# Kernel tuning notes

Measured on AMD Instinct MI355X. Metric: run time of the kernel, lower is better.

Reference implementation:

```python
import jax, jax.numpy as jnp
import numpy as np

N_NODES = 100000
N_EDGES = 1600000
D_FEAT = 128
UNITS = 128
LEAKY_ALPHA = 0.2  # tf.nn.leaky_relu default


def setup_inputs() -> dict:
    key = jax.random.key(0)
    k1, k2, k3, k4 = jax.random.split(key, 4)
    node_states = jax.random.normal(k1, (N_NODES, D_FEAT), dtype=jnp.float32)
    edges = jax.random.randint(k2, (N_EDGES, 2), 0, N_NODES, dtype=jnp.int64)
    kernel = jax.random.normal(k3, (D_FEAT, UNITS), dtype=jnp.float32) * (1.0 / np.sqrt(D_FEAT))
    kernel_attention = jax.random.normal(k4, (2 * UNITS, 1), dtype=jnp.float32) * (1.0 / np.sqrt(2 * UNITS))
    return {
        "node_states": node_states,
        "edges": edges,
        "kernel": kernel,
        "kernel_attention": kernel_attention,
    }


def reference(node_states, edges, kernel, kernel_attention):
    n = node_states.shape[0]
    tgt_idx = edges[:, 0]
    src_idx = edges[:, 1]

    # node_states_transformed: [N, units]
    h = node_states @ kernel

    # Attention logits. concat([tgt, src]) @ ka == tgt @ ka_t + src @ ka_s
    # (avoids materializing the [E, 2*units] concat).
    ka_t = kernel_attention[:UNITS, 0]   # [units]
    ka_s = kernel_attention[UNITS:, 0]   # [units]
    score_t = h @ ka_t                   # [N]
    score_s = h @ ka_s                   # [N]
    e = score_t[tgt_idx] + score_s[src_idx]              # [E]
    e = jax.nn.leaky_relu(e, negative_slope=LEAKY_ALPHA)
    e = jnp.exp(jnp.clip(e, -2.0, 2.0))

    # Segment softmax over incoming edges of each target node.
    sum_e = jax.ops.segment_sum(e, tgt_idx, num_segments=n)  # [N]
    attention = e / (sum_e[tgt_idx] + 1e-9)                  # [E]

    # Weighted scatter-sum of source messages.
    messages = h[src_idx] * attention[:, None]               # [E, units]
    output = jax.ops.segment_sum(messages, tgt_idx, num_segments=n)  # [N, units]
    return output
```

## Files before the change

### kernel.cpp

```cpp
#include <hip/hip_runtime.h>
#include <stdint.h>

typedef unsigned short ushort_t;
typedef __attribute__((ext_vector_type(8))) short short8;
typedef __attribute__((ext_vector_type(4))) float float4v;
typedef __attribute__((ext_vector_type(2))) float float2v;

#define N_NODES 100000
#define N_EDGES 1600000
#define D 128
#define NB_GEMM 1563
#define NBP     782
#define NB_B1   250
#define EPB     6400
#define BUCKETS 782
#define CAP     2560

static __device__ __forceinline__ float2v up2(uint32_t u) {
    float2v r;
    r.x = __builtin_bit_cast(float, u << 16);
    r.y = __builtin_bit_cast(float, u & 0xffff0000u);
    return r;
}
static __device__ __forceinline__ uint32_t f2bf_u(float f) {
    uint32_t u = __builtin_bit_cast(uint32_t, f);
    return (u + 0x7fffu + ((u >> 16) & 1u)) >> 16;
}
static __device__ __forceinline__ ushort_t f2bf(float f) {
    return (ushort_t)f2bf_u(f);
}
static __device__ __forceinline__ uint32_t pack2(float a, float b) {
    return f2bf_u(a) | (f2bf_u(b) << 16);
}
static __device__ __forceinline__ float edge_e(float s) {
    float x = (s >= 0.0f) ? s : 0.2f * s;
    x = fminf(fmaxf(x, -2.0f), 2.0f);
    return __expf(x);
}

__global__ void __launch_bounds__(256) prep_kernel(const float* __restrict__ W,
                                                   const float* __restrict__ KA,
                                                   float* __restrict__ wa,
                                                   ushort_t* __restrict__ WT,
                                                   const int* __restrict__ E,
                                                   int* __restrict__ eflag) {
    __shared__ int s;
    int b = blockIdx.x, t = threadIdx.x;
    int i = b * 256 + t;
    if (b < 64) {
        int k = i >> 7, nn = i & 127;
        int kb = k >> 5, q = (k >> 3) & 3, j = k & 7;
        int tt = nn >> 4, l = nn & 15;
        WT[((kb * 8 + tt) * 64 + q * 16 + l) * 8 + j] = f2bf(W[i]);
    } else if (b == 64) {
        if (t == 0) s = 0;
        __syncthreads();
        int nz = 0;
#pragma unroll
        for (int j = 0; j < 8; j++)
            if (E[(t + j * 256) * 2 + 1] != 0) nz = 1;
        if (nz) atomicOr(&s, 1);
        __syncthreads();
        if (t == 0) *eflag = (s == 0) ? 1 : 0;
    } else if (b == 65) {
        int half = t >> 7, k = t & 127;
        const float* kav = KA + half * 128;
        const float* wrow = W + k * 128;
        float acc = 0.0f;
#pragma unroll 8
        for (int j = 0; j < 128; j++) acc += wrow[j] * kav[j];
        wa[half * 128 + k] = acc;
    }
}

__global__ void __launch_bounds__(256) mega1_kernel(const float* __restrict__ X,
                                                    const ushort_t* __restrict__ WT,
                                                    const float* __restrict__ wa,
                                                    ushort_t* __restrict__ H,
                                                    float* __restrict__ st,
                                                    float* __restrict__ ss,
                                                    int M,
                                                    const int* __restrict__ E,
                                                    const int* __restrict__ eflag,
                                                    int* __restrict__ sortedE,
                                                    ushort_t* __restrict__ bmat,
                                                    ushort_t* __restrict__ lofs) {
    __shared__ int lds_b1[1280];
    if (blockIdx.x >= NBP) {
        int eb = blockIdx.x - NBP;
        int t = threadIdx.x;
        int* lhist = lds_b1;
        int* lpart = lds_b1 + 1024;
        for (int j = t; j < 1024; j += 256) lhist[j] = 0;
        __syncthreads();
        int i64 = *eflag;
        int base = eb * EPB;
        for (int j = 0; j < 25; j++) {
            int i = base + j * 256 + t;
            int tgt = i64 ? E[i * 4] : E[i * 2];
            if ((unsigned)tgt >= (unsigned)N_NODES) tgt = 0;
            atomicAdd(&lhist[tgt >> 7], 1);
        }
        __syncthreads();
        int c0 = lhist[t * 4], c1 = lhist[t * 4 + 1];
        int c2 = lhist[t * 4 + 2], c3 = lhist[t * 4 + 3];
        int sum = c0 + c1 + c2 + c3;
        lpart[t] = sum;
        __syncthreads();
        for (int off = 1; off < 256; off <<= 1) {
            int x = (t >= off) ? lpart[t - off] : 0;
            __syncthreads();
            lpart[t] += x;
            __syncthreads();
        }
        int e0 = lpart[t] - sum;
        int e1 = e0 + c0, e2 = e1 + c1, e3 = e2 + c2;
        int cc[4] = {c0, c1, c2, c3};
        int ee[4] = {e0, e1, e2, e3};
#pragma unroll
        for (int k = 0; k < 4; k++) {
            int bb = t * 4 + k;
            if (bb < BUCKETS) {
                bmat[eb * BUCKETS + bb] = (ushort_t)cc[k];
                lofs[eb * BUCKETS + bb] = (ushort_t)ee[k];
            }
        }
        lhist[t * 4] = e0; lhist[t * 4 + 1] = e1;
        lhist[t * 4 + 2] = e2; lhist[t * 4 + 3] = e3;
        __syncthreads();
        for (int j = 0; j < 25; j++) {
            int i = base + j * 256 + t;
            int tgt, src;
            if (i64) { tgt = E[i * 4]; src = E[i * 4 + 2]; }
            else     { tgt = E[i * 2]; src = E[i * 2 + 1]; }
            if ((unsigned)tgt >= (unsigned)N_NODES) tgt = 0;
            if ((unsigned)src >= (unsigned)N_NODES) src = 0;
            int pos = atomicAdd(&lhist[tgt >> 7], 1);
            if (pos < EPB) sortedE[base + pos] = ((tgt & 127) << 17) | src;
        }
        return;
    }
    int tid = threadIdx.x;
    int wave = tid >> 6, lane = tid & 63;
    int quad = lane >> 4, l16 = lane & 15;
    const short8* Bf = (const short8*)WT;

    int t0 = blockIdx.x;
    int nt = (t0 + NBP < NB_GEMM) ? 2 : 1;

    float4 f[8];
    {
        int ar = t0 * 64 + wave * 16 + l16; if (ar >= M) ar = M - 1;
        const float* xr = X + (size_t)ar * D + quad * 8;
#pragma unroll
        for (int kb = 0; kb < 4; kb++) {
            f[kb * 2]     = *(const float4*)(xr + kb * 32);
            f[kb * 2 + 1] = *(const float4*)(xr + kb * 32 + 4);
        }
    }
    for (int it = 0; it < nt; it++) {
        int m0 = (t0 + it * NBP) * 64 + wave * 16;
        float4 nf[8];
        if (it + 1 < nt) {
            int ar = (t0 + NBP) * 64 + wave * 16 + l16; if (ar >= M) ar = M - 1;
            const float* xr = X + (size_t)ar * D + quad * 8;
#pragma unroll
            for (int kb = 0; kb < 4; kb++) {
                nf[kb * 2]     = *(const float4*)(xr + kb * 32);
                nf[kb * 2 + 1] = *(const float4*)(xr + kb * 32 + 4);
            }
        }
        short8 a[4];
        float sct = 0.0f, scs = 0.0f;
#pragma unroll
        for (int kb = 0; kb < 4; kb++) {
            float4 f0 = f[kb * 2], f1 = f[kb * 2 + 1];
            const float* wt0 = wa + kb * 32 + quad * 8;
            float4 t0v = *(const float4*)(wt0);
            float4 t1v = *(const float4*)(wt0 + 4);
            float4 s0v = *(const float4*)(wt0 + 128);
            float4 s1v = *(const float4*)(wt0 + 132);
            sct += f0.x * t0v.x + f0.y * t0v.y + f0.z * t0v.z + f0.w * t0v.w
                 + f1.x * t1v.x + f1.y * t1v.y + f1.z * t1v.z + f1.w * t1v.w;
            scs += f0.x * s0v.x + f0.y * s0v.y + f0.z * s0v.z + f0.w * s0v.w
                 + f1.x * s1v.x + f1.y * s1v.y + f1.z * s1v.z + f1.w * s1v.w;
            short8 v;
            v[0] = (short)f2bf(f0.x); v[1] = (short)f2bf(f0.y);
            v[2] = (short)f2bf(f0.z); v[3] = (short)f2bf(f0.w);
            v[4] = (short)f2bf(f1.x); v[5] = (short)f2bf(f1.y);
            v[6] = (short)f2bf(f1.z); v[7] = (short)f2bf(f1.w);
            a[kb] = v;
        }
        sct += __shfl_xor(sct, 16); sct += __shfl_xor(sct, 32);
        scs += __shfl_xor(scs, 16); scs += __shfl_xor(scs, 32);
        if (quad == 0 && m0 + l16 < M) { st[m0 + l16] = sct; ss[m0 + l16] = scs; }

        float4v acc[8] = {};
#pragma unroll
        for (int kb = 0; kb < 4; kb++) {
#pragma unroll
            for (int t = 0; t < 8; t++) {
                short8 b = Bf[(kb * 8 + t) * 64 + lane];
                acc[t] = __builtin_amdgcn_mfma_f32_16x16x32_bf16(a[kb], b, acc[t], 0, 0, 0);
            }
        }
#pragma unroll
        for (int r = 0; r < 4; r++) {
            int orow = m0 + quad * 4 + r;
            if (orow < M) {
                uint4 v;
                v.x = pack2(acc[0][r], acc[1][r]);
                v.y = pack2(acc[2][r], acc[3][r]);
                v.z = pack2(acc[4][r], acc[5][r]);
                v.w = pack2(acc[6][r], acc[7][r]);
                *(uint4*)(H + (size_t)orow * D + l16 * 8) = v;
            }
        }
        if (it + 1 < nt) {
#pragma unroll
            for (int j = 0; j < 8; j++) f[j] = nf[j];
        }
    }
}

__global__ void __launch_bounds__(512) agg2_kernel(const ushort_t* __restrict__ bmat,
                                                   const ushort_t* __restrict__ lofs,
                                                   const int* __restrict__ sortedE,
                                                   const float* __restrict__ st,
                                                   const float* __restrict__ ss,
                                                   const ushort_t* __restrict__ H,
                                                   float* __restrict__ out) {
    __shared__ int stage[CAP];
    __shared__ int sortedLoc[CAP];
    __shared__ int lh[128];
    __shared__ int lrp[129];
    __shared__ int wsum[8];
    int b = blockIdx.x, t = threadIdx.x;
    int lane = t & 63, wv = t >> 6;
    int cnt = 0, sst = 0;
    if (t < NB_B1) {
        cnt = bmat[t * BUCKETS + b];
        sst = lofs[t * BUCKETS + b];
    }
    int x = cnt;
#pragma unroll
    for (int off = 1; off < 64; off <<= 1) {
        int y = __shfl_up(x, off);
        if (lane >= off) x += y;
    }
    if (lane == 63) wsum[wv] = x;
    if (t < 128) lh[t] = 0;
    __syncthreads();
    int wbase = 0, total = 0;
#pragma unroll
    for (int w = 0; w < 8; w++) {
        int sv = wsum[w];
        if (w < wv) wbase += sv;
        total += sv;
    }
    if (total > CAP) total = CAP;
    int soff = wbase + x - cnt;
    for (int k = 0; k < cnt; k++) {
        int idx = soff + k;
        if (idx < CAP) stage[idx] = sortedE[t * EPB + sst + k];
    }
    __syncthreads();
    for (int j = t; j < total; j += 512)
        atomicAdd(&lh[stage[j] >> 17], 1);
    __syncthreads();
    int v = (t < 128) ? lh[t] : 0;
    int xs = v;
#pragma unroll
    for (int off = 1; off < 64; off <<= 1) {
        int y = __shfl_up(xs, off);
        if (lane >= off) xs += y;
    }
    if (t == 63) wsum[0] = xs;
    __syncthreads();
    if (t < 128) {
        int inc = (wv == 1) ? xs + wsum[0] : xs;
        int ex = inc - v;
        lrp[t] = ex;
        lh[t]  = ex;
    }
    if (t == 0) lrp[128] = total;
    __syncthreads();
    for (int j = t; j < total; j += 512) {
        int p = stage[j];
        int pos = atomicAdd(&lh[p >> 17], 1);
        if (pos < total) sortedLoc[pos] = p & 0x1FFFF;
    }
    __syncthreads();
    int g = lane >> 4, l = lane & 15;
    for (int nd = wv; nd < 128; nd += 8) {
        int gnode = b * 128 + nd;
        if (gnode >= N_NODES) break;
        int start = lrp[nd], end = lrp[nd + 1];
        float stn = st[gnode];
        float den = 0.0f;
        float2v acc2[4] = {};
        int m = start + g;
        for (; m + 4 < end; m += 8) {
            int s0 = sortedLoc[m], s1 = sortedLoc[m + 4];
            float e0 = edge_e(stn + ss[s0]);
            float e1 = edge_e(stn + ss[s1]);
            den += e0 + e1;
            uint4 p0 = *(const uint4*)(H + ((unsigned)s0 << 7) + l * 8);
            uint4 p1 = *(const uint4*)(H + ((unsigned)s1 << 7) + l * 8);
            float2v E0 = {e0, e0}, E1 = {e1, e1};
            acc2[0] += E0 * up2(p0.x) + E1 * up2(p1.x);
            acc2[1] += E0 * up2(p0.y) + E1 * up2(p1.y);
            acc2[2] += E0 * up2(p0.z) + E1 * up2(p1.z);
            acc2[3] += E0 * up2(p0.w) + E1 * up2(p1.w);
        }
        if (m < end) {
            int s0 = sortedLoc[m];
            float e0 = edge_e(stn + ss[s0]);
            den += e0;
            uint4 p0 = *(const uint4*)(H + ((unsigned)s0 << 7) + l * 8);
            float2v E0 = {e0, e0};
            acc2[0] += E0 * up2(p0.x);
            acc2[1] += E0 * up2(p0.y);
            acc2[2] += E0 * up2(p0.z);
            acc2[3] += E0 * up2(p0.w);
        }
        den += __shfl_xor(den, 16);
        den += __shfl_xor(den, 32);
        float r[8];
#pragma unroll
        for (int j = 0; j < 4; j++) {
            float a0 = acc2[j].x, a1 = acc2[j].y;
            a0 += __shfl_xor(a0, 16); a0 += __shfl_xor(a0, 32);
            a1 += __shfl_xor(a1, 16); a1 += __shfl_xor(a1, 32);
            r[j * 2] = a0; r[j * 2 + 1] = a1;
        }
        float inv = 1.0f / (den + 1e-9f);
        if (g == 0) {
#pragma unroll
            for (int k = 0; k < 8; k++)
                out[(size_t)gnode * D + k * 16 + l] = r[k] * inv;
        }
    }
}

extern "C" void kernel_launch(void* const* d_in, const int* in_sizes, int n_in,
                              void* d_out, int out_size, void* d_ws, size_t ws_size,
                              hipStream_t stream) {
    const float* X  = (const float*)d_in[0];
    const int*   E  = (const int*)d_in[1];
    const float* W  = (const float*)d_in[2];
    const float* KA = (const float*)d_in[3];
    for (int i = 0; i < n_in; i++) {
        int s = in_sizes[i];
        if (s == N_NODES * D)      X  = (const float*)d_in[i];
        else if (s == N_EDGES * 2) E  = (const int*)d_in[i];
        else if (s == D * D)       W  = (const float*)d_in[i];
        else if (s == 2 * D)       KA = (const float*)d_in[i];
    }
    float* out = (float*)d_out;

    char* ws = (char*)d_ws;
    ushort_t* H        = (ushort_t*)(ws + 0);
    float*    wa       = (float*)   (ws + 25600000);
    float*    st       = (float*)   (ws + 25601024);
    float*    ssb      = (float*)   (ws + 26001024);
    int*      sortedE  = (int*)     (ws + 26401024);
    ushort_t* bmat     = (ushort_t*)(ws + 32801024);
    ushort_t* lofs     = (ushort_t*)(ws + 33192032);
    int*      eflag    = (int*)     (ws + 33583040);
    ushort_t* WT       = (ushort_t*)(ws + 33583072);

    prep_kernel<<<66, 256, 0, stream>>>(W, KA, wa, WT, E, eflag);
    mega1_kernel<<<NBP + NB_B1, 256, 0, stream>>>(X, WT, wa, H, st, ssb,
                                                  N_NODES, E, eflag,
                                                  sortedE, bmat, lofs);
    agg2_kernel<<<BUCKETS, 512, 0, stream>>>(bmat, lofs, sortedE, st, ssb,
                                             H, out);
}
```

Before: 227.3 us.

## Split bucketing and GEMM kernels, stage weights in LDS, parallelize staging gather

Splits the fused edge-bucketing/GEMM kernel into two separate launches. The bucketing kernel now reads each edge once with vector loads and keeps bins in registers, and the GEMM stages the transposed weights in LDS. The aggregation kernel fills its staging buffer with one element per thread, finding the owning partition by binary search, and unrolls the gather loop to four edges. The split adds a launch and loses the overlap between bucketing and GEMM, and the larger LDS footprint may cut occupancy.

```diff
diff --git a/kernel.cpp b/kernel.cpp
--- a/kernel.cpp
+++ b/kernel.cpp
@@ -73,78 +73,83 @@
     }
 }
 
-__global__ void __launch_bounds__(256) mega1_kernel(const float* __restrict__ X,
-                                                    const ushort_t* __restrict__ WT,
-                                                    const float* __restrict__ wa,
-                                                    ushort_t* __restrict__ H,
-                                                    float* __restrict__ st,
-                                                    float* __restrict__ ss,
-                                                    int M,
-                                                    const int* __restrict__ E,
-                                                    const int* __restrict__ eflag,
-                                                    int* __restrict__ sortedE,
-                                                    ushort_t* __restrict__ bmat,
-                                                    ushort_t* __restrict__ lofs) {
-    __shared__ int lds_b1[1280];
-    if (blockIdx.x >= NBP) {
-        int eb = blockIdx.x - NBP;
-        int t = threadIdx.x;
-        int* lhist = lds_b1;
-        int* lpart = lds_b1 + 1024;
-        for (int j = t; j < 1024; j += 256) lhist[j] = 0;
+__global__ void __launch_bounds__(256) b1_kernel(const int* __restrict__ E,
+                                                 const int* __restrict__ eflag,
+                                                 int* __restrict__ sortedE,
+                                                 ushort_t* __restrict__ bmat,
+                                                 ushort_t* __restrict__ lofs) {
+    __shared__ int lhist[1024];
+    __shared__ int lpart[256];
+    int eb = blockIdx.x, t = threadIdx.x;
+    for (int j = t; j < 1024; j += 256) lhist[j] = 0;
+    __syncthreads();
+    int i64 = *eflag;
+    int base = eb * EPB;
+    int bin[25], w[25];
+#pragma unroll
+    for (int j = 0; j < 25; j++) {
+        int i = base + j * 256 + t;
+        int tgt, src;
+        if (i64) { uint4 v = *(const uint4*)(E + (size_t)i * 4); tgt = (int)v.x; src = (int)v.z; }
+        else     { uint2 v = *(const uint2*)(E + (size_t)i * 2); tgt = (int)v.x; src = (int)v.y; }
+        if ((unsigned)tgt >= (unsigned)N_NODES) tgt = 0;
+        if ((unsigned)src >= (unsigned)N_NODES) src = 0;
+        bin[j] = tgt >> 7;
+        w[j]   = ((tgt & 127) << 17) | src;
+        atomicAdd(&lhist[bin[j]], 1);
+    }
+    __syncthreads();
+    int c0 = lhist[t * 4], c1 = lhist[t * 4 + 1];
+    int c2 = lhist[t * 4 + 2], c3 = lhist[t * 4 + 3];
+    int sum = c0 + c1 + c2 + c3;
+    lpart[t] = sum;
+    __syncthreads();
+    for (int off = 1; off < 256; off <<= 1) {
+        int x = (t >= off) ? lpart[t - off] : 0;
         __syncthreads();
-        int i64 = *eflag;
-        int base = eb * EPB;
-        for (int j = 0; j < 25; j++) {
-            int i = base + j * 256 + t;
-            int tgt = i64 ? E[i * 4] : E[i * 2];
-            if ((unsigned)tgt >= (unsigned)N_NODES) tgt = 0;
-            atomicAdd(&lhist[tgt >> 7], 1);
-        }
+        lpart[t] += x;
         __syncthreads();
-        int c0 = lhist[t * 4], c1 = lhist[t * 4 + 1];
-        int c2 = lhist[t * 4 + 2], c3 = lhist[t * 4 + 3];
-        int sum = c0 + c1 + c2 + c3;
-        lpart[t] = sum;
-        __syncthreads();
-        for (int off = 1; off < 256; off <<= 1) {
-            int x = (t >= off) ? lpart[t - off] : 0;
-            __syncthreads();
-            lpart[t] += x;
-            __syncthreads();
-        }
-        int e0 = lpart[t] - sum;
-        int e1 = e0 + c0, e2 = e1 + c1, e3 = e2 + c2;
-        int cc[4] = {c0, c1, c2, c3};
-        int ee[4] = {e0, e1, e2, e3};
-#pragma unroll
-        for (int k = 0; k < 4; k++) {
-            int bb = t * 4 + k;
-            if (bb < BUCKETS) {
-                bmat[eb * BUCKETS + bb] = (ushort_t)cc[k];
-                lofs[eb * BUCKETS + bb] = (ushort_t)ee[k];
-            }
-        }
-        lhist[t * 4] = e0; lhist[t * 4 + 1] = e1;
-        lhist[t * 4 + 2] = e2; lhist[t * 4 + 3] = e3;
-        __syncthreads();
-        for (int j = 0; j < 25; j++) {
-            int i = base + j * 256 + t;
-            int tgt, src;
-            if (i64) { tgt = E[i * 4]; src = E[i * 4 + 2]; }
-            else     { tgt = E[i * 2]; src = E[i * 2 + 1]; }
-            if ((unsigned)tgt >= (unsigned)N_NODES) tgt = 0;
-            if ((unsigned)src >= (unsigned)N_NODES) src = 0;
-            int pos = atomicAdd(&lhist[tgt >> 7], 1);
-            if (pos < EPB) sortedE[base + pos] = ((tgt & 127) << 17) | src;
-        }
-        return;
-    }
+    }
+    int e0 = lpart[t] - sum;
+    int e1 = e0 + c0, e2 = e1 + c1, e3 = e2 + c2;
+    int cc[4] = {c0, c1, c2, c3};
+    int ee[4] = {e0, e1, e2, e3};
+#pragma unroll
+    for (int k = 0; k < 4; k++) {
+        int bb = t * 4 + k;
+        if (bb < BUCKETS) {
+            bmat[eb * BUCKETS + bb] = (ushort_t)cc[k];
+            lofs[eb * BUCKETS + bb] = (ushort_t)ee[k];
+        }
+    }
+    lhist[t * 4] = e0; lhist[t * 4 + 1] = e1;
+    lhist[t * 4 + 2] = e2; lhist[t * 4 + 3] = e3;
+    __syncthreads();
+#pragma unroll
+    for (int j = 0; j < 25; j++) {
+        int pos = atomicAdd(&lhist[bin[j]], 1);
+        if (pos < EPB) sortedE[base + pos] = w[j];
+    }
+}
+
+__global__ void __launch_bounds__(256) gemm_kernel(const float* __restrict__ X,
+                                                   const ushort_t* __restrict__ WT,
+                                                   const float* __restrict__ wa,
+                                                   ushort_t* __restrict__ H,
+                                                   float* __restrict__ st,
+                                                   float* __restrict__ ss,
+                                                   int M) {
+    __shared__ ushort_t lds_wt[16384];
     int tid = threadIdx.x;
+    {
+        const uint4* srcp = (const uint4*)WT;
+        uint4* dstp = (uint4*)lds_wt;
+        for (int j = tid; j < 2048; j += 256) dstp[j] = srcp[j];
+    }
+    __syncthreads();
+
     int wave = tid >> 6, lane = tid & 63;
     int quad = lane >> 4, l16 = lane & 15;
-    const short8* Bf = (const short8*)WT;
-
     int t0 = blockIdx.x;
     int nt = (t0 + NBP < NB_GEMM) ? 2 : 1;
 
@@ -200,7 +205,7 @@
         for (int kb = 0; kb < 4; kb++) {
 #pragma unroll
             for (int t = 0; t < 8; t++) {
-                short8 b = Bf[(kb * 8 + t) * 64 + lane];
+                short8 b = *(const short8*)(&lds_wt[((kb * 8 + t) * 64 + lane) * 8]);
                 acc[t] = __builtin_amdgcn_mfma_f32_16x16x32_bf16(a[kb], b, acc[t], 0, 0, 0);
             }
         }
@@ -235,6 +240,8 @@
     __shared__ int lh[128];
     __shared__ int lrp[129];
     __shared__ int wsum[8];
+    __shared__ int lsoff[NB_B1];
+    __shared__ int lsst[NB_B1];
     int b = blockIdx.x, t = threadIdx.x;
     int lane = t & 63, wv = t >> 6;
     int cnt = 0, sst = 0;
@@ -260,9 +267,15 @@
     }
     if (total > CAP) total = CAP;
     int soff = wbase + x - cnt;
-    for (int k = 0; k < cnt; k++) {
-        int idx = soff + k;
-        if (idx < CAP) stage[idx] = sortedE[t * EPB + sst + k];
+    if (t < NB_B1) { lsoff[t] = soff; lsst[t] = sst; }
+    __syncthreads();
+    for (int j = t; j < total; j += 512) {
+        int lo = 0, hi = NB_B1 - 1;
+        while (lo < hi) {
+            int mid = (lo + hi + 1) >> 1;
+            if (lsoff[mid] <= j) lo = mid; else hi = mid - 1;
+        }
+        stage[j] = sortedE[lo * EPB + lsst[lo] + (j - lsoff[lo])];
     }
     __syncthreads();
     for (int j = t; j < total; j += 512)
@@ -300,6 +313,24 @@
         float den = 0.0f;
         float2v acc2[4] = {};
         int m = start + g;
+        for (; m + 12 < end; m += 16) {
+            int s0 = sortedLoc[m],     s1 = sortedLoc[m + 4];
+            int s2 = sortedLoc[m + 8], s3 = sortedLoc[m + 12];
+            float e0 = edge_e(stn + ss[s0]);
+            float e1 = edge_e(stn + ss[s1]);
+            float e2 = edge_e(stn + ss[s2]);
+            float e3 = edge_e(stn + ss[s3]);
+            den += (e0 + e1) + (e2 + e3);
+            uint4 p0 = *(const uint4*)(H + ((unsigned)s0 << 7) + l * 8);
+            uint4 p1 = *(const uint4*)(H + ((unsigned)s1 << 7) + l * 8);
+            uint4 p2 = *(const uint4*)(H + ((unsigned)s2 << 7) + l * 8);
+            uint4 p3 = *(const uint4*)(H + ((unsigned)s3 << 7) + l * 8);
+            float2v E0 = {e0, e0}, E1 = {e1, e1}, E2 = {e2, e2}, E3 = {e3, e3};
+            acc2[0] += E0 * up2(p0.x) + E1 * up2(p1.x) + E2 * up2(p2.x) + E3 * up2(p3.x);
+            acc2[1] += E0 * up2(p0.y) + E1 * up2(p1.y) + E2 * up2(p2.y) + E3 * up2(p3.y);
+            acc2[2] += E0 * up2(p0.z) + E1 * up2(p1.z) + E2 * up2(p2.z) + E3 * up2(p3.z);
+            acc2[3] += E0 * up2(p0.w) + E1 * up2(p1.w) + E2 * up2(p2.w) + E3 * up2(p3.w);
+        }
         for (; m + 4 < end; m += 8) {
             int s0 = sortedLoc[m], s1 = sortedLoc[m + 4];
             float e0 = edge_e(stn + ss[s0]);
@@ -371,9 +402,8 @@
     ushort_t* WT       = (ushort_t*)(ws + 33583072);
 
     prep_kernel<<<66, 256, 0, stream>>>(W, KA, wa, WT, E, eflag);
-    mega1_kernel<<<NBP + NB_B1, 256, 0, stream>>>(X, WT, wa, H, st, ssb,
-                                                  N_NODES, E, eflag,
-                                                  sortedE, bmat, lofs);
+    b1_kernel<<<NB_B1, 256, 0, stream>>>(E, eflag, sortedE, bmat, lofs);
+    gemm_kernel<<<NBP, 256, 0, stream>>>(X, WT, wa, H, st, ssb, N_NODES);
     agg2_kernel<<<BUCKETS, 512, 0, stream>>>(bmat, lofs, sortedE, st, ssb,
                                              H, out);
 }
```

Measured after the change: 213.7 us. 6.0% less time.
